# Kernel tuning notes

Hardware: AMD Instinct MI355X
Metric: run time of the kernel (lower is better)

Reference implementation:

```python
import jax, jax.numpy as jnp
import numpy as np

INPUT_DIM = 256
OUTPUT_DIM = 512
NUM_KNOTS = 64
RANGE_KNOTS = (-1.0, 1.0)
DEGREE = 3
BATCH = 4096


def bspline_basis(x, knots, degree):
    """Cox-de Boor recursion. x: [B, I], knots: [K] (uniform, ascending).
    Returns basis values [B, I, K - degree - 1]."""
    xe = x[..., None]  # [B, I, 1]
    # degree-0: indicator of knot interval k, k = 0..K-2
    basis = ((xe >= knots[:-1]) & (xe < knots[1:])).astype(x.dtype)  # [B, I, K-1]
    for d in range(1, degree + 1):
        k = np.arange(knots.shape[0] - d - 1)
        left = (xe - knots[k]) / (knots[k + d] - knots[k]) * basis[..., :-1]
        right = (knots[k + d + 1] - xe) / (knots[k + d + 1] - knots[k + 1]) * basis[..., 1:]
        basis = left + right  # [B, I, K-d-1]
    return basis


def setup_inputs() -> dict:
    key = jax.random.key(0)
    kx, kb, ks = jax.random.split(key, 3)
    x = jax.random.uniform(kx, (BATCH, INPUT_DIM), dtype=jnp.float32)
    wb = jax.random.uniform(kb, (INPUT_DIM, OUTPUT_DIM), dtype=jnp.float32)
    ws = jax.random.uniform(ks, (INPUT_DIM, OUTPUT_DIM), dtype=jnp.float32)
    cps = jnp.ones((INPUT_DIM, NUM_KNOTS), dtype=jnp.float32)
    knots = jnp.asarray(np.linspace(RANGE_KNOTS[0], RANGE_KNOTS[1], NUM_KNOTS), dtype=jnp.float32)
    return {"x": x, "wb": wb, "ws": ws, "cps": cps, "knots": knots}


def reference(x, wb, ws, cps, knots):
    num_basis = NUM_KNOTS - DEGREE - 1
    basis = bspline_basis(x, knots, DEGREE)            # [B, I, num_basis]
    # per-input-dim spline value: sum_k cps[i, k] * B_k(x[b, i])
    spline = jnp.einsum('bik,ik->bi', basis, cps[:, :num_basis])  # [B, I]
    base = jax.nn.silu(x)                               # [B, I]
    # out[b, o] = sum_i wb[i, o] * silu(x[b, i]) + ws[i, o] * spline[b, i]
    out = base @ wb + spline @ ws                       # [B, O]
    return out
```

## Files before the change

### kernel.cpp

```cpp
#include <hip/hip_runtime.h>
#include <hip/hip_bf16.h>

#define BATCH    4096
#define IN_DIM   256
#define OUT_DIM  512
#define KDIM     512
#define NKNOTS   64
#define NBASIS   60

typedef __attribute__((ext_vector_type(8))) short bf16x8;
typedef __attribute__((ext_vector_type(4))) float f32x4;

__device__ __align__(16) short g_A [BATCH   * KDIM];
__device__ __align__(16) short g_Bt[OUT_DIM * KDIM];

__device__ __forceinline__ short f2bf(float f) {
    __hip_bfloat16 h = __float2bfloat16(f);
    return *reinterpret_cast<short*>(&h);
}

#define NBLK_A 512
#define NBLK_B 64

__global__ __launch_bounds__(256) void prep_kernel(
        const float* __restrict__ x, const float* __restrict__ wb,
        const float* __restrict__ ws, const float* __restrict__ cps) {
    __shared__ float T[64][65];

    if (blockIdx.x < NBLK_A) {
        const int g  = blockIdx.x * 256 + threadIdx.x;
        const int b  = g >> 5;
        const int i0 = (g & 31) << 3;
        float xv[8];
        *(f32x4*)&xv[0] = *(const f32x4*)&x[b * IN_DIM + i0];
        *(f32x4*)&xv[4] = *(const f32x4*)&x[b * IN_DIM + i0 + 4];
        bf16x8 sil, spl;
        #pragma unroll
        for (int e = 0; e < 8; ++e) {
            float v = xv[e];
            float s = v / (1.0f + __expf(-v));
            float u  = (v + 1.0f) * 31.5f;
            float fj = floorf(u);
            int   j  = (int)fj;
            float sp = 0.0f;
            if (j >= 0 && j <= 62) {
                float t  = u - fj;
                float t2 = t * t, t3 = t2 * t;
                float omt = 1.0f - t;
                const float c6 = 1.0f / 6.0f;
                float w0 = omt * omt * omt * c6;
                float w1 = (3.0f*t3 - 6.0f*t2 + 4.0f) * c6;
                float w2 = (-3.0f*t3 + 3.0f*t2 + 3.0f*t + 1.0f) * c6;
                float w3 = t3 * c6;
                const float* cp = cps + (i0 + e) * NKNOTS;
                int k0 = j - 3;
                if (k0     >= 0 && k0     < NBASIS) sp += w0 * cp[k0];
                if (k0 + 1 >= 0 && k0 + 1 < NBASIS) sp += w1 * cp[k0 + 1];
                if (k0 + 2 >= 0 && k0 + 2 < NBASIS) sp += w2 * cp[k0 + 2];
                if (               k0 + 3 < NBASIS) sp += w3 * cp[k0 + 3];
            }
            sil[e] = f2bf(s);
            spl[e] = f2bf(sp);
        }
        *(bf16x8*)&g_A[b * KDIM + i0]          = sil;
        *(bf16x8*)&g_A[b * KDIM + IN_DIM + i0] = spl;
    } else {
        const int bb = blockIdx.x - NBLK_A;
        const int k0 = (bb >> 3) * 64;
        const int n0 = (bb & 7) * 64;
        const float* W = (k0 < IN_DIM) ? wb + (size_t)k0 * OUT_DIM
                                       : ws + (size_t)(k0 - IN_DIM) * OUT_DIM;
        const int t  = threadIdx.x;
        const int r  = t >> 2;
        const int c0 = (t & 3) * 16;
        #pragma unroll
        for (int e = 0; e < 16; e += 4) {
            f32x4 v = *(const f32x4*)&W[r * OUT_DIM + n0 + c0 + e];
            T[r][c0 + e + 0] = v[0];
            T[r][c0 + e + 1] = v[1];
            T[r][c0 + e + 2] = v[2];
            T[r][c0 + e + 3] = v[3];
        }
        __syncthreads();
        short tmp[16];
        #pragma unroll
        for (int e = 0; e < 16; ++e) tmp[e] = f2bf(T[c0 + e][r]);
        *(bf16x8*)&g_Bt[(n0 + r) * KDIM + k0 + c0]     = *(bf16x8*)&tmp[0];
        *(bf16x8*)&g_Bt[(n0 + r) * KDIM + k0 + c0 + 8] = *(bf16x8*)&tmp[8];
    }
}

__global__ __launch_bounds__(256) void gemm_kernel(float* __restrict__ C) {
    const int bid  = blockIdx.x;
    const int sbid = (bid & 7) * 64 + (bid >> 3);
    const int m0   = (sbid >> 3) * 64;
    const int n0   = (sbid & 7) * 64;
    const int tid  = threadIdx.x;
    const int lane = tid & 63;
    const int wave = tid >> 6;
    const int wm   = (wave & 1) * 32;
    const int wn   = (wave >> 1) * 32;
    const int fr   = lane & 15;
    const int koff = (lane >> 4) * 8;

    const short* A0 = g_A  + (size_t)(m0 + wm + fr) * KDIM + koff;
    const short* A1 = A0 + 16 * KDIM;
    const short* B0 = g_Bt + (size_t)(n0 + wn + fr) * KDIM + koff;
    const short* B1 = B0 + 16 * KDIM;

    f32x4 acc[2][2] = {};
    #pragma unroll 4
    for (int k = 0; k < KDIM; k += 32) {
        bf16x8 a0 = *(const bf16x8*)(A0 + k);
        bf16x8 a1 = *(const bf16x8*)(A1 + k);
        bf16x8 b0 = *(const bf16x8*)(B0 + k);
        bf16x8 b1 = *(const bf16x8*)(B1 + k);
        acc[0][0] = __builtin_amdgcn_mfma_f32_16x16x32_bf16(a0, b0, acc[0][0], 0, 0, 0);
        acc[0][1] = __builtin_amdgcn_mfma_f32_16x16x32_bf16(a0, b1, acc[0][1], 0, 0, 0);
        acc[1][0] = __builtin_amdgcn_mfma_f32_16x16x32_bf16(a1, b0, acc[1][0], 0, 0, 0);
        acc[1][1] = __builtin_amdgcn_mfma_f32_16x16x32_bf16(a1, b1, acc[1][1], 0, 0, 0);
    }

    const int rbase = (lane >> 4) * 4;
    #pragma unroll
    for (int mt = 0; mt < 2; ++mt) {
        #pragma unroll
        for (int nt = 0; nt < 2; ++nt) {
            #pragma unroll
            for (int r = 0; r < 4; ++r) {
                int row = m0 + wm + mt * 16 + rbase + r;
                int col = n0 + wn + nt * 16 + fr;
                C[row * OUT_DIM + col] = acc[mt][nt][r];
            }
        }
    }
}

extern "C" void kernel_launch(void* const* d_in, const int* in_sizes, int n_in,
                              void* d_out, int out_size, void* d_ws, size_t ws_size,
                              hipStream_t stream) {
    (void)in_sizes; (void)n_in; (void)d_ws; (void)ws_size; (void)out_size;
    const float* x   = (const float*)d_in[0];
    const float* wb  = (const float*)d_in[1];
    const float* wsp = (const float*)d_in[2];
    const float* cps = (const float*)d_in[3];
    float* out = (float*)d_out;

    prep_kernel<<<NBLK_A + NBLK_B, 256, 0, stream>>>(x, wb, wsp, cps);
    gemm_kernel<<<512, 256, 0, stream>>>(out);
}
```

Baseline: 87.78 us.

## Stage GEMM A/B tiles through padded LDS with coalesced cooperative loads

```diff
diff --git a/kernel.cpp b/kernel.cpp
--- a/kernel.cpp
+++ b/kernel.cpp
@@ -90,7 +90,15 @@
     }
 }
 
+#define BM 64
+#define BN 64
+#define BK 128
+#define LDSS 136
+
 __global__ __launch_bounds__(256) void gemm_kernel(float* __restrict__ C) {
+    __shared__ __align__(16) short As[BM * LDSS];
+    __shared__ __align__(16) short Bs[BN * LDSS];
+
     const int bid  = blockIdx.x;
     const int sbid = (bid & 7) * 64 + (bid >> 3);
     const int m0   = (sbid >> 3) * 64;
@@ -103,22 +111,30 @@
     const int fr   = lane & 15;
     const int koff = (lane >> 4) * 8;
 
-    const short* A0 = g_A  + (size_t)(m0 + wm + fr) * KDIM + koff;
-    const short* A1 = A0 + 16 * KDIM;
-    const short* B0 = g_Bt + (size_t)(n0 + wn + fr) * KDIM + koff;
-    const short* B1 = B0 + 16 * KDIM;
+    f32x4 acc[2][2] = {};
 
-    f32x4 acc[2][2] = {};
-    #pragma unroll 4
-    for (int k = 0; k < KDIM; k += 32) {
-        bf16x8 a0 = *(const bf16x8*)(A0 + k);
-        bf16x8 a1 = *(const bf16x8*)(A1 + k);
-        bf16x8 b0 = *(const bf16x8*)(B0 + k);
-        bf16x8 b1 = *(const bf16x8*)(B1 + k);
-        acc[0][0] = __builtin_amdgcn_mfma_f32_16x16x32_bf16(a0, b0, acc[0][0], 0, 0, 0);
-        acc[0][1] = __builtin_amdgcn_mfma_f32_16x16x32_bf16(a0, b1, acc[0][1], 0, 0, 0);
-        acc[1][0] = __builtin_amdgcn_mfma_f32_16x16x32_bf16(a1, b0, acc[1][0], 0, 0, 0);
-        acc[1][1] = __builtin_amdgcn_mfma_f32_16x16x32_bf16(a1, b1, acc[1][1], 0, 0, 0);
+    for (int k0 = 0; k0 < KDIM; k0 += BK) {
+        #pragma unroll
+        for (int s = 0; s < 4; ++s) {
+            const int c = tid + s * 256;
+            const int r = c >> 4, o = (c & 15) * 8;
+            *(uint4*)&As[r * LDSS + o] = *(const uint4*)&g_A [(m0 + r) * KDIM + k0 + o];
+            *(uint4*)&Bs[r * LDSS + o] = *(const uint4*)&g_Bt[(n0 + r) * KDIM + k0 + o];
+        }
+        __syncthreads();
+
+        #pragma unroll
+        for (int kk = 0; kk < BK; kk += 32) {
+            bf16x8 a0 = *(const bf16x8*)&As[(wm + fr)      * LDSS + kk + koff];
+            bf16x8 a1 = *(const bf16x8*)&As[(wm + 16 + fr) * LDSS + kk + koff];
+            bf16x8 b0 = *(const bf16x8*)&Bs[(wn + fr)      * LDSS + kk + koff];
+            bf16x8 b1 = *(const bf16x8*)&Bs[(wn + 16 + fr) * LDSS + kk + koff];
+            acc[0][0] = __builtin_amdgcn_mfma_f32_16x16x32_bf16(a0, b0, acc[0][0], 0, 0, 0);
+            acc[0][1] = __builtin_amdgcn_mfma_f32_16x16x32_bf16(a0, b1, acc[0][1], 0, 0, 0);
+            acc[1][0] = __builtin_amdgcn_mfma_f32_16x16x32_bf16(a1, b0, acc[1][0], 0, 0, 0);
+            acc[1][1] = __builtin_amdgcn_mfma_f32_16x16x32_bf16(a1, b1, acc[1][1], 0, 0, 0);
+        }
+        __syncthreads();
     }
 
     const int rbase = (lane >> 4) * 4;
```

New measurement: 78.04 us. -11.1%, faster.
